# Performance work log

Hardware: AMD Instinct MI355X
Metric: run time of the kernel (lower is better)

The kernel has to match this reference:

```python
import jax, jax.numpy as jnp
import numpy as np

CH = 256
CQK = CH // 8
B, H, W = 4, 64, 64


def setup_inputs() -> dict:
    key = jax.random.key(0)
    ks = jax.random.split(key, 8)
    s_qk = 1.0 / np.sqrt(CH)  # MSR init for 1x1 conv: std = 1/sqrt(fan_in)
    x = jax.random.normal(ks[0], (B, CH, H, W), dtype=jnp.float32)
    Wq = jax.random.normal(ks[1], (CQK, CH), dtype=jnp.float32) * s_qk
    bq = jnp.zeros((CQK,), dtype=jnp.float32)
    Wk = jax.random.normal(ks[2], (CQK, CH), dtype=jnp.float32) * s_qk
    bk = jnp.zeros((CQK,), dtype=jnp.float32)
    Wv = jax.random.normal(ks[3], (CH, CH), dtype=jnp.float32) * s_qk
    bv = jnp.zeros((CH,), dtype=jnp.float32)
    # NOTE: module inits gamma=0; use a nonzero value so the attention branch is active
    gamma = jnp.float32(0.5) * jnp.ones((1,), dtype=jnp.float32)
    return {"x": x, "Wq": Wq, "bq": bq, "Wk": Wk, "bk": bk, "Wv": Wv, "bv": bv, "gamma": gamma}


def reference(x, Wq, bq, Wk, bk, Wv, bv, gamma):
    b, c, h, w = x.shape
    n = h * w
    xf = x.reshape(b, c, n)  # [B, C, N]
    # 1x1 convs are per-pixel channel projections
    q = jnp.einsum('oc,bcn->bon', Wq, xf) + bq[:, None]  # [B, C/8, N]
    k = jnp.einsum('oc,bcn->bon', Wk, xf) + bk[:, None]  # [B, C/8, N]
    v = jnp.einsum('oc,bcn->bon', Wv, xf) + bv[:, None]  # [B, C, N]
    # scores[b, i, j] = q[:, i] . k[:, j]  (no scaling, as in source)
    att = jax.nn.softmax(jnp.einsum('bci,bcj->bij', q, k), axis=-1)  # [B, N, N]
    out = jnp.einsum('bcj,bij->bci', v, att).reshape(b, c, h, w)
    return x + gamma[0] * out
```

## Files before the change

### kernel.cpp

```cpp
#include <hip/hip_runtime.h>
#include <hip/hip_bf16.h>

typedef unsigned short u16;
typedef __attribute__((ext_vector_type(8))) __bf16 bf16x8;
typedef __attribute__((ext_vector_type(8))) unsigned short u16x8;
typedef __attribute__((ext_vector_type(4))) float f32x4;
typedef __attribute__((ext_vector_type(16))) float f32x16;
typedef __attribute__((ext_vector_type(4))) unsigned int u32x4;
typedef __attribute__((ext_vector_type(2))) unsigned int u32x2;

#define MFMA16(a, b, c) __builtin_amdgcn_mfma_f32_16x16x32_bf16((a), (b), (c), 0, 0, 0)
#define MFMA32(a, b, c) __builtin_amdgcn_mfma_f32_32x32x16_bf16((a), (b), (c), 0, 0, 0)

#define BN 4
#define CH 256
#define CQK 32
#define NPIX 4096

__device__ __forceinline__ u16 f2bf(float f) {
    __hip_bfloat16 h = __float2bfloat16(f);
    return *reinterpret_cast<u16*>(&h);
}

__device__ __forceinline__ unsigned pack2(float a, float b) {
    return (unsigned)f2bf(a) | ((unsigned)f2bf(b) << 16);
}

__device__ __forceinline__ unsigned packtr(float a, float b) {
    return __builtin_amdgcn_perm(__float_as_uint(b), __float_as_uint(a), 0x07060302u);
}

__device__ __forceinline__ float bf2f(u16 v) {
    return __uint_as_float(((unsigned)v) << 16);
}

__device__ __forceinline__ f32x16 zero16() {
    f32x16 z;
#pragma unroll
    for (int i = 0; i < 16; ++i) z[i] = 0.f;
    return z;
}

__device__ __forceinline__ int perm16(int k) {
    return (k & 3) | ((k & 4) << 1) | ((k & 8) >> 1);
}

__global__ void k_transpose(const float* __restrict__ x, u16* __restrict__ xt) {
    __shared__ float xs[64][65];
    int n0 = blockIdx.x * 64, c0 = blockIdx.y * 64, b = blockIdx.z;
    int t = threadIdx.x;
    const float* xp = x + ((size_t)(b * CH + c0)) * NPIX + n0;
#pragma unroll
    for (int it = 0; it < 16; ++it) {
        int idx = it * 256 + t;
        int cc = idx >> 6, nn = idx & 63;
        xs[cc][nn] = xp[(size_t)cc * NPIX + nn];
    }
    __syncthreads();
    u16* op = xt + ((size_t)(b * NPIX + n0)) * CH + c0;
#pragma unroll
    for (int it = 0; it < 16; ++it) {
        int idx = it * 256 + t;
        int nn = idx >> 6, cc = idx & 63;
        op[(size_t)nn * CH + cc] = f2bf(xs[cc][nn]);
    }
}

__global__ void k_wcvt(const float* __restrict__ Wq, const float* __restrict__ Wk,
                       const float* __restrict__ Wv, u16* __restrict__ Wbf) {
    int idx = blockIdx.x * 256 + threadIdx.x;
    int o = idx >> 8, c = idx & 255;
    float v;
    if (o < 32) v = Wq[o * 256 + c];
    else if (o < 64) v = Wk[(o - 32) * 256 + c];
    else v = Wv[(o - 64) * 256 + c];
    Wbf[idx] = f2bf(v);
}

__launch_bounds__(256, 1)
__global__ void k_proj(const u16* __restrict__ Wbf, const u16* __restrict__ xt,
                       const float* __restrict__ bq, const float* __restrict__ bk,
                       const float* __restrict__ bv,
                       u16* __restrict__ qb, u16* __restrict__ kb, u16* __restrict__ vb) {
    int b = blockIdx.y, n0 = blockIdx.x * 64;
    int t = threadIdx.x, w = t >> 6, l = t & 63;
    int lr = l & 15, lg = l >> 4;

    f32x4 acc[5][4];
#pragma unroll
    for (int s = 0; s < 5; ++s)
#pragma unroll
        for (int u = 0; u < 4; ++u) acc[s][u] = f32x4{0.f, 0.f, 0.f, 0.f};

    const u16* xtb = xt + ((size_t)(b * NPIX + n0)) * CH;

#pragma unroll
    for (int kk = 0; kk < 8; ++kk) {
        int kof = kk * 32 + lg * 8;
        bf16x8 af[5], bfr[4];
#pragma unroll
        for (int s = 0; s < 5; ++s) {
            int o = w * 16 + s * 64 + lr;
            af[s] = *reinterpret_cast<const bf16x8*>(Wbf + (size_t)o * 256 + kof);
        }
#pragma unroll
        for (int u = 0; u < 4; ++u) {
            int n = u * 16 + lr;
            bfr[u] = *reinterpret_cast<const bf16x8*>(xtb + (size_t)n * CH + kof);
        }
#pragma unroll
        for (int s = 0; s < 5; ++s)
#pragma unroll
            for (int u = 0; u < 4; ++u) acc[s][u] = MFMA16(af[s], bfr[u], acc[s][u]);
    }

    int lrp = perm16(lr);
#pragma unroll
    for (int s = 0; s < 5; ++s) {
        int o0 = w * 16 + s * 64;
#pragma unroll
        for (int r = 0; r < 4; ++r) {
            int o = o0 + lg * 4 + r;
            float bias = (o < 32) ? bq[o] : (o < 64) ? bk[o - 32] : bv[o - 64];
#pragma unroll
            for (int u = 0; u < 4; ++u) {
                float val = acc[s][u][r] + bias;
                u16 h = f2bf(val);
                if (o < 32) qb[((size_t)b * NPIX + n0 + u * 16 + lr) * CQK + o] = h;
                else if (o < 64) kb[((size_t)b * NPIX + n0 + u * 16 + lr) * CQK + (o - 32)] = h;
                else {
                    int c = o - 64;
                    int jp = (u & 1) * 16 + lrp;
                    int sl = jp >> 3, off = jp & 7;
                    int jps = ((sl ^ ((c >> 1) & 3)) << 3) | off;
                    vb[((size_t)(b * CH + c)) * NPIX + n0 + (u >> 1) * 32 + jps] = h;
                }
            }
        }
    }
}

template <int NCHUNK>
__launch_bounds__(128, 2)
__global__ void k_attn8(const u16* __restrict__ qb, const u16* __restrict__ kb,
                        const u16* __restrict__ vb, const float* __restrict__ x,
                        const float* __restrict__ gamma,
                        u16* __restrict__ pacc, float* __restrict__ plsum,
                        float* __restrict__ out) {
    constexpr int JCH = NPIX / NCHUNK;
    constexpr int NT = JCH / 32;
    int it = blockIdx.x;
    int sc = blockIdx.y;
    int s = sc >> 1, ch = sc & 1;
    int b = blockIdx.z;
    int t = threadIdx.x, w = t >> 6, l = t & 63;
    int lr = l & 31, hi = l >> 5;
    int i0 = it * 128 + w * 64;
    int j0 = s * JCH;

    __shared__ alignas(16) u16 vlds[3][4096];
    __shared__ float lsl[2][64];

    bf16x8 qf[2][2];
#pragma unroll
    for (int is = 0; is < 2; ++is) {
        const u16* qrow = qb + ((size_t)b * NPIX + i0 + is * 32 + lr) * CQK;
        qf[is][0] = *(const bf16x8*)(qrow + hi * 8);
        qf[is][1] = *(const bf16x8*)(qrow + 16 + hi * 8);
    }

    const u16* kbase = kb + (size_t)b * NPIX * CQK;
    const u16* vsrc =
        vb + ((size_t)(b * CH + ch * 128 + w * 64 + (l >> 2))) * NPIX + j0 + (l & 3) * 8;

    f32x16 acc[2][4];
#pragma unroll
    for (int is = 0; is < 2; ++is)
#pragma unroll
        for (int ct = 0; ct < 4; ++ct) acc[is][ct] = zero16();
    float lsum[2] = {0.f, 0.f};

    bf16x8 kc0, kc1;
    auto kload = [&](int tt) {
        const u16* kr = kbase + (size_t)(j0 + tt * 32 + lr) * CQK;
        kc0 = *(const bf16x8*)(kr + hi * 8);
        kc1 = *(const bf16x8*)(kr + 16 + hi * 8);
    };
    auto dma = [&](int buf, int tt) {
#pragma unroll
        for (int mm = 0; mm < 4; ++mm) {
            const u16* src = vsrc + (size_t)mm * 16 * NPIX + tt * 32;
            __builtin_amdgcn_global_load_lds(
                (const __attribute__((address_space(1))) unsigned int*)src,
                (__attribute__((address_space(3))) unsigned int*)(
                    &vlds[buf][(w * 64 + mm * 16) * 32]),
                16, 0, 0);
        }
    };
    auto qkexp = [&](bf16x8 (&pa)[4]) {
#pragma unroll
        for (int is = 0; is < 2; ++is) {
            f32x16 sf = MFMA32(kc0, qf[is][0], zero16());
            sf = MFMA32(kc1, qf[is][1], sf);
            float P[16];
#pragma unroll
            for (int e = 0; e < 16; ++e) {
                P[e] = __expf(sf[e] - 32.0f);
                lsum[is] += P[e];
            }
            u32x4 wa = {packtr(P[0], P[1]), packtr(P[2], P[3]),
                        packtr(P[4], P[5]), packtr(P[6], P[7])};
            u32x4 wc = {packtr(P[8], P[9]), packtr(P[10], P[11]),
                        packtr(P[12], P[13]), packtr(P[14], P[15])};
            pa[is * 2] = __builtin_bit_cast(bf16x8, wa);
            pa[is * 2 + 1] = __builtin_bit_cast(bf16x8, wc);
        }
    };
    auto pv = [&](int buf, bf16x8 (&pa)[4]) {
        const u16* base = &vlds[buf][0];
#pragma unroll
        for (int ct = 0; ct < 4; ++ct) {
            int row = ct * 32 + lr;
            int key = (row >> 1) & 3;
            const u16* rp = base + row * 32;
            bf16x8 vf0 = *(const bf16x8*)(rp + ((hi ^ key) << 3));
            bf16x8 vf1 = *(const bf16x8*)(rp + (((2 + hi) ^ key) << 3));
#pragma unroll
            for (int is = 0; is < 2; ++is) {
                acc[is][ct] = MFMA32(pa[is * 2], vf0, acc[is][ct]);
                acc[is][ct] = MFMA32(pa[is * 2 + 1], vf1, acc[is][ct]);
            }
        }
    };

    bf16x8 paA[4], paB[4];

    dma(0, 0);
    kload(0);
    qkexp(paA);
    kload(1);

    for (int tt = 0; tt < NT - 1; ++tt) {
        dma((tt + 1) % 3, tt + 1);
        qkexp(paB);
        kload(tt + 2 < NT ? tt + 2 : NT - 1);
        asm volatile("s_waitcnt vmcnt(6)" ::: "memory");
        __builtin_amdgcn_s_barrier();
        __builtin_amdgcn_sched_barrier(0);
        pv(tt % 3, paA);
#pragma unroll
        for (int e = 0; e < 4; ++e) paA[e] = paB[e];
    }
    asm volatile("s_waitcnt vmcnt(0)" ::: "memory");
    __builtin_amdgcn_s_barrier();
    __builtin_amdgcn_sched_barrier(0);
    pv((NT - 1) % 3, paA);

    lsum[0] += __shfl_xor(lsum[0], 32);
    lsum[1] += __shfl_xor(lsum[1], 32);

    if constexpr (NCHUNK == 1) {
        float g = gamma[0];
        if (l < 32) {
            lsl[w][l] = g / lsum[0];
        }
        if (l >= 32) lsl[w][l] = 0.f;
        if (l < 32) lsl[w][32 + l] = g / lsum[1];
        asm volatile("s_waitcnt lgkmcnt(0)" ::: "memory");
#pragma unroll
        for (int is = 0; is < 2; ++is)
#pragma unroll
            for (int ct = 0; ct < 4; ++ct) {
                int c = ch * 128 + ct * 32 + lr;
                const float* xp = x + ((size_t)(b * CH + c)) * NPIX + i0;
                float* op = out + ((size_t)(b * CH + c)) * NPIX + i0;
#pragma unroll
                for (int r = 0; r < 16; ++r) {
                    int il = is * 32 + (r & 3) + 8 * (r >> 2) + 4 * hi;
                    op[il] = xp[il] + acc[is][ct][r] * lsl[w][il];
                }
            }
    } else {
        size_t pbase = ((((size_t)s * BN + b) * 32 + it) * 256) * 128;
#pragma unroll
        for (int is = 0; is < 2; ++is)
#pragma unroll
            for (int ct = 0; ct < 4; ++ct) {
                int c = ch * 128 + ct * 32 + lr;
#pragma unroll
                for (int q = 0; q < 4; ++q) {
                    int il0 = w * 64 + is * 32 + 8 * q + 4 * hi;
                    u32x2 pr = {pack2(acc[is][ct][4 * q], acc[is][ct][4 * q + 1]),
                                pack2(acc[is][ct][4 * q + 2], acc[is][ct][4 * q + 3])};
                    *(u32x2*)(pacc + pbase + (size_t)c * 128 + il0) = pr;
                }
            }
        if (ch == 0 && l < 32) {
            size_t lb = (((size_t)s * BN + b) * 32 + it) * 128 + w * 64;
            plsum[lb + l] = lsum[0];
            plsum[lb + 32 + l] = lsum[1];
        }
    }
}

template <int NCHUNK>
__global__ void k_reduce(const u16* __restrict__ pacc, const float* __restrict__ plsum,
                         const float* __restrict__ x, const float* __restrict__ gamma,
                         float* __restrict__ out) {
    int cg = blockIdx.x, it = blockIdx.y, b = blockIdx.z;
    int t = threadIdx.x;
    int c0 = cg * 32;
    __shared__ float invl[128];

    if (t < 128) {
        float lt = 0.f;
#pragma unroll
        for (int s = 0; s < NCHUNK; ++s)
            lt += plsum[(((size_t)s * BN + b) * 32 + it) * 128 + t];
        invl[t] = gamma[0] / lt;
    }
    __syncthreads();

    const size_t chunk_stride = (size_t)BN * 32 * 256 * 128;
    size_t base = (((size_t)b * 32 + it) * 256 + c0) * 128;

#pragma unroll
    for (int k = 0; k < 2; ++k) {
        int v = k * 256 + t;
        int cl = v >> 4;
        int io = (v & 15) * 8;
        size_t off = base + (size_t)cl * 128 + io;
        f32x4 a0 = {0.f, 0.f, 0.f, 0.f}, a1 = a0;
#pragma unroll
        for (int s = 0; s < NCHUNK; ++s) {
            u16x8 p = *(const u16x8*)(pacc + (size_t)s * chunk_stride + off);
            a0[0] += bf2f(p[0]); a0[1] += bf2f(p[1]); a0[2] += bf2f(p[2]); a0[3] += bf2f(p[3]);
            a1[0] += bf2f(p[4]); a1[1] += bf2f(p[5]); a1[2] += bf2f(p[6]); a1[3] += bf2f(p[7]);
        }
        f32x4 i0v = *(const f32x4*)(&invl[io]);
        f32x4 i1v = *(const f32x4*)(&invl[io + 4]);
        size_t oi = ((size_t)(b * CH + c0 + cl)) * NPIX + it * 128 + io;
        f32x4 x0 = *(const f32x4*)(x + oi);
        f32x4 x1 = *(const f32x4*)(x + oi + 4);
        *(f32x4*)(out + oi) = x0 + a0 * i0v;
        *(f32x4*)(out + oi + 4) = x1 + a1 * i1v;
    }
}

extern "C" void kernel_launch(void* const* d_in, const int* in_sizes, int n_in,
                              void* d_out, int out_size, void* d_ws, size_t ws_size,
                              hipStream_t stream) {
    const float* x = (const float*)d_in[0];
    const float* Wq = (const float*)d_in[1];
    const float* bq = (const float*)d_in[2];
    const float* Wk = (const float*)d_in[3];
    const float* bk = (const float*)d_in[4];
    const float* Wv = (const float*)d_in[5];
    const float* bv = (const float*)d_in[6];
    const float* gamma = (const float*)d_in[7];
    float* out = (float*)d_out;

    char* ws = (char*)d_ws;
    u16* xt = (u16*)(ws);
    u16* Wbf = (u16*)(ws + 8388608);
    u16* qb = (u16*)(ws + 8388608 + 163840);
    u16* kb = (u16*)(ws + 8388608 + 163840 + 1048576);
    u16* vb = (u16*)(ws + 8388608 + 163840 + 2097152);
    const size_t base_end = 8388608 + 163840 + 2097152 + 8388608;
    u16* pacc = (u16*)(ws + base_end);

    hipLaunchKernelGGL(k_transpose, dim3(64, 4, 4), dim3(256), 0, stream, x, xt);
    hipLaunchKernelGGL(k_wcvt, dim3(320), dim3(256), 0, stream, Wq, Wk, Wv, Wbf);
    hipLaunchKernelGGL(k_proj, dim3(64, 4), dim3(256), 0, stream, Wbf, xt, bq, bk, bv, qb, kb, vb);

    const size_t pacc4 = (size_t)4 * BN * NPIX * CH * 2;
    const size_t pls4 = (size_t)4 * BN * NPIX * 4;

    if (ws_size >= base_end + pacc4 + pls4) {
        float* plsum = (float*)(ws + base_end + pacc4);
        hipLaunchKernelGGL(k_attn8<4>, dim3(32, 8, 4), dim3(128), 0, stream,
                           qb, kb, vb, x, gamma, pacc, plsum, out);
        hipLaunchKernelGGL(k_reduce<4>, dim3(8, 32, 4), dim3(256), 0, stream,
                           pacc, plsum, x, gamma, out);
    } else {
        hipLaunchKernelGGL(k_attn8<1>, dim3(32, 2, 4), dim3(128), 0, stream,
                           qb, kb, vb, x, gamma, pacc, (float*)pacc, out);
    }
}
```

Measured before the change: 94.57 us.

## Halve query rows per wave, use exp2 with prescaled Q, widen V swizzle

The attention kernel now processes 32 query rows per wave instead of 64, doubling the grid and raising launch bounds to 3 blocks per CU. The goal is fewer accumulator registers and more occupancy to hide the latency of K/V loads and exp. Q is prescaled by log2(e) in the projection so the softmax uses exp2f with an equivalent shift. The V LDS swizzle changes from 8-element to 4-element granularity over 8 slots, with reads done as 64-bit pieces. The cost is that K/V tiles are reloaded and re-DMA'd twice as often per query, and each MFMA pair now reuses its V operand fragments less.

```diff
diff --git a/kernel.cpp b/kernel.cpp
--- a/kernel.cpp
+++ b/kernel.cpp
@@ -16,6 +16,9 @@
 #define CH 256
 #define CQK 32
 #define NPIX 4096
+
+#define LOG2E 1.44269504088896f
+#define SHIFT2 46.1662413084468f
 
 __device__ __forceinline__ u16 f2bf(float f) {
     __hip_bfloat16 h = __float2bfloat16(f);
@@ -125,15 +128,16 @@
 #pragma unroll
             for (int u = 0; u < 4; ++u) {
                 float val = acc[s][u][r] + bias;
-                u16 h = f2bf(val);
-                if (o < 32) qb[((size_t)b * NPIX + n0 + u * 16 + lr) * CQK + o] = h;
-                else if (o < 64) kb[((size_t)b * NPIX + n0 + u * 16 + lr) * CQK + (o - 32)] = h;
-                else {
+                if (o < 32) {
+                    qb[((size_t)b * NPIX + n0 + u * 16 + lr) * CQK + o] = f2bf(val * LOG2E);
+                } else if (o < 64) {
+                    kb[((size_t)b * NPIX + n0 + u * 16 + lr) * CQK + (o - 32)] = f2bf(val);
+                } else {
                     int c = o - 64;
                     int jp = (u & 1) * 16 + lrp;
-                    int sl = jp >> 3, off = jp & 7;
-                    int jps = ((sl ^ ((c >> 1) & 3)) << 3) | off;
-                    vb[((size_t)(b * CH + c)) * NPIX + n0 + (u >> 1) * 32 + jps] = h;
+                    int s8 = jp >> 2, rem = jp & 3;
+                    int jps = ((s8 ^ ((c >> 1) & 7)) << 2) | rem;
+                    vb[((size_t)(b * CH + c)) * NPIX + n0 + (u >> 1) * 32 + jps] = f2bf(val);
                 }
             }
         }
@@ -141,44 +145,38 @@
 }
 
 template <int NCHUNK>
-__launch_bounds__(128, 2)
-__global__ void k_attn8(const u16* __restrict__ qb, const u16* __restrict__ kb,
+__launch_bounds__(128, 3)
+__global__ void k_attn9(const u16* __restrict__ qb, const u16* __restrict__ kb,
                         const u16* __restrict__ vb, const float* __restrict__ x,
                         const float* __restrict__ gamma,
                         u16* __restrict__ pacc, float* __restrict__ plsum,
                         float* __restrict__ out) {
     constexpr int JCH = NPIX / NCHUNK;
     constexpr int NT = JCH / 32;
-    int it = blockIdx.x;
+    int itp = blockIdx.x;
     int sc = blockIdx.y;
     int s = sc >> 1, ch = sc & 1;
     int b = blockIdx.z;
     int t = threadIdx.x, w = t >> 6, l = t & 63;
     int lr = l & 31, hi = l >> 5;
-    int i0 = it * 128 + w * 64;
+    int i0 = itp * 64 + w * 32;
     int j0 = s * JCH;
 
     __shared__ alignas(16) u16 vlds[3][4096];
-    __shared__ float lsl[2][64];
-
-    bf16x8 qf[2][2];
-#pragma unroll
-    for (int is = 0; is < 2; ++is) {
-        const u16* qrow = qb + ((size_t)b * NPIX + i0 + is * 32 + lr) * CQK;
-        qf[is][0] = *(const bf16x8*)(qrow + hi * 8);
-        qf[is][1] = *(const bf16x8*)(qrow + 16 + hi * 8);
-    }
+    __shared__ float lsl[2][32];
+
+    const u16* qrow = qb + ((size_t)b * NPIX + i0 + lr) * CQK;
+    bf16x8 qf0 = *(const bf16x8*)(qrow + hi * 8);
+    bf16x8 qf1 = *(const bf16x8*)(qrow + 16 + hi * 8);
 
     const u16* kbase = kb + (size_t)b * NPIX * CQK;
     const u16* vsrc =
         vb + ((size_t)(b * CH + ch * 128 + w * 64 + (l >> 2))) * NPIX + j0 + (l & 3) * 8;
 
-    f32x16 acc[2][4];
-#pragma unroll
-    for (int is = 0; is < 2; ++is)
-#pragma unroll
-        for (int ct = 0; ct < 4; ++ct) acc[is][ct] = zero16();
-    float lsum[2] = {0.f, 0.f};
+    f32x16 acc[4];
+#pragma unroll
+    for (int ct = 0; ct < 4; ++ct) acc[ct] = zero16();
+    float lsum = 0.f;
 
     bf16x8 kc0, kc1;
     auto kload = [&](int tt) {
@@ -197,108 +195,99 @@
                 16, 0, 0);
         }
     };
-    auto qkexp = [&](bf16x8 (&pa)[4]) {
-#pragma unroll
-        for (int is = 0; is < 2; ++is) {
-            f32x16 sf = MFMA32(kc0, qf[is][0], zero16());
-            sf = MFMA32(kc1, qf[is][1], sf);
-            float P[16];
-#pragma unroll
-            for (int e = 0; e < 16; ++e) {
-                P[e] = __expf(sf[e] - 32.0f);
-                lsum[is] += P[e];
-            }
-            u32x4 wa = {packtr(P[0], P[1]), packtr(P[2], P[3]),
-                        packtr(P[4], P[5]), packtr(P[6], P[7])};
-            u32x4 wc = {packtr(P[8], P[9]), packtr(P[10], P[11]),
-                        packtr(P[12], P[13]), packtr(P[14], P[15])};
-            pa[is * 2] = __builtin_bit_cast(bf16x8, wa);
-            pa[is * 2 + 1] = __builtin_bit_cast(bf16x8, wc);
-        }
+    auto qkexp = [&](bf16x8& pa0, bf16x8& pa1) {
+        f32x16 sf = MFMA32(kc0, qf0, zero16());
+        sf = MFMA32(kc1, qf1, sf);
+        float P[16];
+#pragma unroll
+        for (int e = 0; e < 16; ++e) {
+            P[e] = exp2f(sf[e] - SHIFT2);
+            lsum += P[e];
+        }
+        u32x4 wa = {packtr(P[0], P[1]), packtr(P[2], P[3]),
+                    packtr(P[4], P[5]), packtr(P[6], P[7])};
+        u32x4 wc = {packtr(P[8], P[9]), packtr(P[10], P[11]),
+                    packtr(P[12], P[13]), packtr(P[14], P[15])};
+        pa0 = __builtin_bit_cast(bf16x8, wa);
+        pa1 = __builtin_bit_cast(bf16x8, wc);
     };
-    auto pv = [&](int buf, bf16x8 (&pa)[4]) {
+    auto pv = [&](int buf, bf16x8 pa0, bf16x8 pa1) {
         const u16* base = &vlds[buf][0];
 #pragma unroll
         for (int ct = 0; ct < 4; ++ct) {
             int row = ct * 32 + lr;
-            int key = (row >> 1) & 3;
-            const u16* rp = base + row * 32;
-            bf16x8 vf0 = *(const bf16x8*)(rp + ((hi ^ key) << 3));
-            bf16x8 vf1 = *(const bf16x8*)(rp + (((2 + hi) ^ key) << 3));
-#pragma unroll
-            for (int is = 0; is < 2; ++is) {
-                acc[is][ct] = MFMA32(pa[is * 2], vf0, acc[is][ct]);
-                acc[is][ct] = MFMA32(pa[is * 2 + 1], vf1, acc[is][ct]);
-            }
+            int key = (row >> 1) & 7;
+            const u32x2* rp = (const u32x2*)(base + row * 32);
+            u32x2 e0 = rp[(2 * hi) ^ key];
+            u32x2 e1 = rp[(2 * hi + 1) ^ key];
+            u32x2 e2 = rp[(4 + 2 * hi) ^ key];
+            u32x2 e3 = rp[(5 + 2 * hi) ^ key];
+            u32x4 v0 = {e0[0], e0[1], e1[0], e1[1]};
+            u32x4 v1 = {e2[0], e2[1], e3[0], e3[1]};
+            bf16x8 vf0 = __builtin_bit_cast(bf16x8, v0);
+            bf16x8 vf1 = __builtin_bit_cast(bf16x8, v1);
+            acc[ct] = MFMA32(pa0, vf0, acc[ct]);
+            acc[ct] = MFMA32(pa1, vf1, acc[ct]);
         }
     };
 
-    bf16x8 paA[4], paB[4];
+    bf16x8 paA0, paA1, paB0, paB1;
 
     dma(0, 0);
     kload(0);
-    qkexp(paA);
+    qkexp(paA0, paA1);
     kload(1);
 
     for (int tt = 0; tt < NT - 1; ++tt) {
         dma((tt + 1) % 3, tt + 1);
-        qkexp(paB);
+        qkexp(paB0, paB1);
         kload(tt + 2 < NT ? tt + 2 : NT - 1);
         asm volatile("s_waitcnt vmcnt(6)" ::: "memory");
         __builtin_amdgcn_s_barrier();
         __builtin_amdgcn_sched_barrier(0);
-        pv(tt % 3, paA);
-#pragma unroll
-        for (int e = 0; e < 4; ++e) paA[e] = paB[e];
+        pv(tt % 3, paA0, paA1);
+        paA0 = paB0;
+        paA1 = paB1;
     }
     asm volatile("s_waitcnt vmcnt(0)" ::: "memory");
     __builtin_amdgcn_s_barrier();
     __builtin_amdgcn_sched_barrier(0);
-    pv((NT - 1) % 3, paA);
-
-    lsum[0] += __shfl_xor(lsum[0], 32);
-    lsum[1] += __shfl_xor(lsum[1], 32);
+    pv((NT - 1) % 3, paA0, paA1);
+
+    lsum += __shfl_xor(lsum, 32);
 
     if constexpr (NCHUNK == 1) {
         float g = gamma[0];
-        if (l < 32) {
-            lsl[w][l] = g / lsum[0];
-        }
-        if (l >= 32) lsl[w][l] = 0.f;
-        if (l < 32) lsl[w][32 + l] = g / lsum[1];
+        if (l < 32) lsl[w][l] = g / lsum;
         asm volatile("s_waitcnt lgkmcnt(0)" ::: "memory");
-#pragma unroll
-        for (int is = 0; is < 2; ++is)
-#pragma unroll
-            for (int ct = 0; ct < 4; ++ct) {
-                int c = ch * 128 + ct * 32 + lr;
-                const float* xp = x + ((size_t)(b * CH + c)) * NPIX + i0;
-                float* op = out + ((size_t)(b * CH + c)) * NPIX + i0;
-#pragma unroll
-                for (int r = 0; r < 16; ++r) {
-                    int il = is * 32 + (r & 3) + 8 * (r >> 2) + 4 * hi;
-                    op[il] = xp[il] + acc[is][ct][r] * lsl[w][il];
-                }
+        __builtin_amdgcn_s_barrier();
+#pragma unroll
+        for (int ct = 0; ct < 4; ++ct) {
+            int c = ch * 128 + ct * 32 + lr;
+            const float* xp = x + ((size_t)(b * CH + c)) * NPIX + i0;
+            float* op = out + ((size_t)(b * CH + c)) * NPIX + i0;
+#pragma unroll
+            for (int r = 0; r < 16; ++r) {
+                int il = (r & 3) + 8 * (r >> 2) + 4 * hi;
+                op[il] = xp[il] + acc[ct][r] * lsl[w][il];
             }
+        }
     } else {
-        size_t pbase = ((((size_t)s * BN + b) * 32 + it) * 256) * 128;
-#pragma unroll
-        for (int is = 0; is < 2; ++is)
-#pragma unroll
-            for (int ct = 0; ct < 4; ++ct) {
-                int c = ch * 128 + ct * 32 + lr;
-#pragma unroll
-                for (int q = 0; q < 4; ++q) {
-                    int il0 = w * 64 + is * 32 + 8 * q + 4 * hi;
-                    u32x2 pr = {pack2(acc[is][ct][4 * q], acc[is][ct][4 * q + 1]),
-                                pack2(acc[is][ct][4 * q + 2], acc[is][ct][4 * q + 3])};
-                    *(u32x2*)(pacc + pbase + (size_t)c * 128 + il0) = pr;
-                }
+        size_t pbase = ((((size_t)s * BN + b) * 32 + (itp >> 1)) * 256) * 128;
+        int ibase = (itp & 1) * 64 + w * 32;
+#pragma unroll
+        for (int ct = 0; ct < 4; ++ct) {
+            int c = ch * 128 + ct * 32 + lr;
+#pragma unroll
+            for (int q = 0; q < 4; ++q) {
+                int il0 = ibase + 8 * q + 4 * hi;
+                u32x2 pr = {pack2(acc[ct][4 * q], acc[ct][4 * q + 1]),
+                            pack2(acc[ct][4 * q + 2], acc[ct][4 * q + 3])};
+                *(u32x2*)(pacc + pbase + (size_t)c * 128 + il0) = pr;
             }
+        }
         if (ch == 0 && l < 32) {
-            size_t lb = (((size_t)s * BN + b) * 32 + it) * 128 + w * 64;
-            plsum[lb + l] = lsum[0];
-            plsum[lb + 32 + l] = lsum[1];
+            plsum[(((size_t)s * BN + b) * 32 + (itp >> 1)) * 128 + ibase + l] = lsum;
         }
     }
 }
@@ -378,12 +367,12 @@
 
     if (ws_size >= base_end + pacc4 + pls4) {
         float* plsum = (float*)(ws + base_end + pacc4);
-        hipLaunchKernelGGL(k_attn8<4>, dim3(32, 8, 4), dim3(128), 0, stream,
+        hipLaunchKernelGGL(k_attn9<4>, dim3(64, 8, 4), dim3(128), 0, stream,
                            qb, kb, vb, x, gamma, pacc, plsum, out);
         hipLaunchKernelGGL(k_reduce<4>, dim3(8, 32, 4), dim3(256), 0, stream,
                            pacc, plsum, x, gamma, out);
     } else {
-        hipLaunchKernelGGL(k_attn8<1>, dim3(32, 2, 4), dim3(128), 0, stream,
+        hipLaunchKernelGGL(k_attn9<1>, dim3(64, 2, 4), dim3(128), 0, stream,
                            qb, kb, vb, x, gamma, pacc, (float*)pacc, out);
     }
 }
```

Measured after the change: 120.7 us. 1.28x slower.

## Double attention j-tile to 64 with double-buffered V LDS and 8-way swizzle

Applied to the files above, without the earlier changes.

The attention kernel now processes 64 keys per iteration instead of 32. The V tile moves from a triple buffer to a double buffer of twice the size, with a barrier at the end of each iteration. The V layout written by the projection kernel changes to an 8-group XOR swizzle at 4-element granularity, and the PV loop reads V as 8-byte pieces. Raising wave priority around the PV MFMAs with s_setprio aims to cut loop overhead and barrier count per key. The trade-off is losing the previous one-tile-ahead softmax overlap and adding a second barrier each iteration.

```diff
diff --git a/kernel.cpp b/kernel.cpp
--- a/kernel.cpp
+++ b/kernel.cpp
@@ -131,8 +131,8 @@
                 else {
                     int c = o - 64;
                     int jp = (u & 1) * 16 + lrp;
-                    int sl = jp >> 3, off = jp & 7;
-                    int jps = ((sl ^ ((c >> 1) & 3)) << 3) | off;
+                    int s8 = jp >> 2, rem = jp & 3;
+                    int jps = ((s8 ^ ((c >> 1) & 7)) << 2) | rem;
                     vb[((size_t)(b * CH + c)) * NPIX + n0 + (u >> 1) * 32 + jps] = h;
                 }
             }
@@ -142,13 +142,13 @@
 
 template <int NCHUNK>
 __launch_bounds__(128, 2)
-__global__ void k_attn8(const u16* __restrict__ qb, const u16* __restrict__ kb,
-                        const u16* __restrict__ vb, const float* __restrict__ x,
-                        const float* __restrict__ gamma,
-                        u16* __restrict__ pacc, float* __restrict__ plsum,
-                        float* __restrict__ out) {
+__global__ void k_attn10(const u16* __restrict__ qb, const u16* __restrict__ kb,
+                         const u16* __restrict__ vb, const float* __restrict__ x,
+                         const float* __restrict__ gamma,
+                         u16* __restrict__ pacc, float* __restrict__ plsum,
+                         float* __restrict__ out) {
     constexpr int JCH = NPIX / NCHUNK;
-    constexpr int NT = JCH / 32;
+    constexpr int NT = JCH / 64;
     int it = blockIdx.x;
     int sc = blockIdx.y;
     int s = sc >> 1, ch = sc & 1;
@@ -158,7 +158,7 @@
     int i0 = it * 128 + w * 64;
     int j0 = s * JCH;
 
-    __shared__ alignas(16) u16 vlds[3][4096];
+    __shared__ alignas(16) u16 vlds[2][8192];
     __shared__ float lsl[2][64];
 
     bf16x8 qf[2][2];
@@ -170,103 +170,116 @@
     }
 
     const u16* kbase = kb + (size_t)b * NPIX * CQK;
-    const u16* vsrc =
-        vb + ((size_t)(b * CH + ch * 128 + w * 64 + (l >> 2))) * NPIX + j0 + (l & 3) * 8;
+    const u16* vsrc = vb + ((size_t)(b * CH + ch * 128 + w * 64 + (l >> 3))) * NPIX +
+                      j0 + ((l >> 2) & 1) * 32 + (l & 3) * 8;
 
     f32x16 acc[2][4];
 #pragma unroll
     for (int is = 0; is < 2; ++is)
 #pragma unroll
         for (int ct = 0; ct < 4; ++ct) acc[is][ct] = zero16();
-    float lsum[2] = {0.f, 0.f};
-
-    bf16x8 kc0, kc1;
+    float lsum[2][2] = {{0.f, 0.f}, {0.f, 0.f}};
+
+    bf16x8 kc[4];
     auto kload = [&](int tt) {
-        const u16* kr = kbase + (size_t)(j0 + tt * 32 + lr) * CQK;
-        kc0 = *(const bf16x8*)(kr + hi * 8);
-        kc1 = *(const bf16x8*)(kr + 16 + hi * 8);
+#pragma unroll
+        for (int jsub = 0; jsub < 2; ++jsub) {
+            const u16* kr = kbase + (size_t)(j0 + tt * 64 + jsub * 32 + lr) * CQK;
+            kc[2 * jsub] = *(const bf16x8*)(kr + hi * 8);
+            kc[2 * jsub + 1] = *(const bf16x8*)(kr + 16 + hi * 8);
+        }
     };
     auto dma = [&](int buf, int tt) {
 #pragma unroll
-        for (int mm = 0; mm < 4; ++mm) {
-            const u16* src = vsrc + (size_t)mm * 16 * NPIX + tt * 32;
+        for (int mm = 0; mm < 8; ++mm) {
+            const u16* src = vsrc + (size_t)mm * 8 * NPIX + tt * 64;
             __builtin_amdgcn_global_load_lds(
                 (const __attribute__((address_space(1))) unsigned int*)src,
                 (__attribute__((address_space(3))) unsigned int*)(
-                    &vlds[buf][(w * 64 + mm * 16) * 32]),
+                    &vlds[buf][(w * 64 + mm * 8) * 64]),
                 16, 0, 0);
         }
     };
-    auto qkexp = [&](bf16x8 (&pa)[4]) {
-#pragma unroll
-        for (int is = 0; is < 2; ++is) {
-            f32x16 sf = MFMA32(kc0, qf[is][0], zero16());
-            sf = MFMA32(kc1, qf[is][1], sf);
-            float P[16];
-#pragma unroll
-            for (int e = 0; e < 16; ++e) {
-                P[e] = __expf(sf[e] - 32.0f);
-                lsum[is] += P[e];
+    auto qkexp = [&](bf16x8 (&pa)[2][4]) {
+#pragma unroll
+        for (int jsub = 0; jsub < 2; ++jsub)
+#pragma unroll
+            for (int is = 0; is < 2; ++is) {
+                f32x16 sf = MFMA32(kc[2 * jsub], qf[is][0], zero16());
+                sf = MFMA32(kc[2 * jsub + 1], qf[is][1], sf);
+                float P[16];
+#pragma unroll
+                for (int e = 0; e < 16; ++e) {
+                    P[e] = __expf(sf[e] - 32.0f);
+                    lsum[is][jsub] += P[e];
+                }
+                u32x4 wa = {packtr(P[0], P[1]), packtr(P[2], P[3]),
+                            packtr(P[4], P[5]), packtr(P[6], P[7])};
+                u32x4 wc = {packtr(P[8], P[9]), packtr(P[10], P[11]),
+                            packtr(P[12], P[13]), packtr(P[14], P[15])};
+                pa[jsub][is * 2] = __builtin_bit_cast(bf16x8, wa);
+                pa[jsub][is * 2 + 1] = __builtin_bit_cast(bf16x8, wc);
             }
-            u32x4 wa = {packtr(P[0], P[1]), packtr(P[2], P[3]),
-                        packtr(P[4], P[5]), packtr(P[6], P[7])};
-            u32x4 wc = {packtr(P[8], P[9]), packtr(P[10], P[11]),
-                        packtr(P[12], P[13]), packtr(P[14], P[15])};
-            pa[is * 2] = __builtin_bit_cast(bf16x8, wa);
-            pa[is * 2 + 1] = __builtin_bit_cast(bf16x8, wc);
-        }
     };
-    auto pv = [&](int buf, bf16x8 (&pa)[4]) {
+    auto pv = [&](int buf, bf16x8 (&pa)[2][4]) {
         const u16* base = &vlds[buf][0];
-#pragma unroll
-        for (int ct = 0; ct < 4; ++ct) {
-            int row = ct * 32 + lr;
-            int key = (row >> 1) & 3;
-            const u16* rp = base + row * 32;
-            bf16x8 vf0 = *(const bf16x8*)(rp + ((hi ^ key) << 3));
-            bf16x8 vf1 = *(const bf16x8*)(rp + (((2 + hi) ^ key) << 3));
-#pragma unroll
-            for (int is = 0; is < 2; ++is) {
-                acc[is][ct] = MFMA32(pa[is * 2], vf0, acc[is][ct]);
-                acc[is][ct] = MFMA32(pa[is * 2 + 1], vf1, acc[is][ct]);
+        __builtin_amdgcn_s_setprio(1);
+#pragma unroll
+        for (int jsub = 0; jsub < 2; ++jsub)
+#pragma unroll
+            for (int ct = 0; ct < 4; ++ct) {
+                int row = ct * 32 + lr;
+                int key = (row >> 1) & 7;
+                const u32x2* rp = (const u32x2*)(base + row * 64 + jsub * 32);
+                u32x2 e0 = rp[(2 * hi) ^ key];
+                u32x2 e1 = rp[(2 * hi + 1) ^ key];
+                u32x2 e2 = rp[(4 + 2 * hi) ^ key];
+                u32x2 e3 = rp[(5 + 2 * hi) ^ key];
+                u32x4 v0 = {e0[0], e0[1], e1[0], e1[1]};
+                u32x4 v1 = {e2[0], e2[1], e3[0], e3[1]};
+                bf16x8 vf0 = __builtin_bit_cast(bf16x8, v0);
+                bf16x8 vf1 = __builtin_bit_cast(bf16x8, v1);
+#pragma unroll
+                for (int is = 0; is < 2; ++is) {
+                    acc[is][ct] = MFMA32(pa[jsub][is * 2], vf0, acc[is][ct]);
+                    acc[is][ct] = MFMA32(pa[jsub][is * 2 + 1], vf1, acc[is][ct]);
+                }
             }
-        }
+        __builtin_amdgcn_s_setprio(0);
     };
-
-    bf16x8 paA[4], paB[4];
 
     dma(0, 0);
     kload(0);
-    qkexp(paA);
-    kload(1);
-
-    for (int tt = 0; tt < NT - 1; ++tt) {
-        dma((tt + 1) % 3, tt + 1);
-        qkexp(paB);
-        kload(tt + 2 < NT ? tt + 2 : NT - 1);
-        asm volatile("s_waitcnt vmcnt(6)" ::: "memory");
+
+    for (int tt = 0; tt < NT; ++tt) {
+        bf16x8 pa[2][4];
+        if (tt + 1 < NT) dma((tt + 1) & 1, tt + 1);
+        qkexp(pa);
+        if (tt + 1 < NT) kload(tt + 1);
+        if (tt + 1 < NT) {
+            asm volatile("s_waitcnt vmcnt(12)" ::: "memory");
+        } else {
+            asm volatile("s_waitcnt vmcnt(0)" ::: "memory");
+        }
         __builtin_amdgcn_s_barrier();
         __builtin_amdgcn_sched_barrier(0);
-        pv(tt % 3, paA);
-#pragma unroll
-        for (int e = 0; e < 4; ++e) paA[e] = paB[e];
-    }
-    asm volatile("s_waitcnt vmcnt(0)" ::: "memory");
-    __builtin_amdgcn_s_barrier();
-    __builtin_amdgcn_sched_barrier(0);
-    pv((NT - 1) % 3, paA);
-
-    lsum[0] += __shfl_xor(lsum[0], 32);
-    lsum[1] += __shfl_xor(lsum[1], 32);
+        pv(tt & 1, pa);
+        __builtin_amdgcn_s_barrier();
+    }
+
+    float ls0 = lsum[0][0] + lsum[0][1];
+    float ls1 = lsum[1][0] + lsum[1][1];
+    ls0 += __shfl_xor(ls0, 32);
+    ls1 += __shfl_xor(ls1, 32);
 
     if constexpr (NCHUNK == 1) {
         float g = gamma[0];
         if (l < 32) {
-            lsl[w][l] = g / lsum[0];
-        }
-        if (l >= 32) lsl[w][l] = 0.f;
-        if (l < 32) lsl[w][32 + l] = g / lsum[1];
+            lsl[w][l] = g / ls0;
+            lsl[w][32 + l] = g / ls1;
+        }
         asm volatile("s_waitcnt lgkmcnt(0)" ::: "memory");
+        __builtin_amdgcn_s_barrier();
 #pragma unroll
         for (int is = 0; is < 2; ++is)
 #pragma unroll
@@ -297,8 +310,8 @@
             }
         if (ch == 0 && l < 32) {
             size_t lb = (((size_t)s * BN + b) * 32 + it) * 128 + w * 64;
-            plsum[lb + l] = lsum[0];
-            plsum[lb + 32 + l] = lsum[1];
+            plsum[lb + l] = ls0;
+            plsum[lb + 32 + l] = ls1;
         }
     }
 }
@@ -378,12 +391,12 @@
 
     if (ws_size >= base_end + pacc4 + pls4) {
         float* plsum = (float*)(ws + base_end + pacc4);
-        hipLaunchKernelGGL(k_attn8<4>, dim3(32, 8, 4), dim3(128), 0, stream,
+        hipLaunchKernelGGL(k_attn10<4>, dim3(32, 8, 4), dim3(128), 0, stream,
                            qb, kb, vb, x, gamma, pacc, plsum, out);
         hipLaunchKernelGGL(k_reduce<4>, dim3(8, 32, 4), dim3(256), 0, stream,
                            pacc, plsum, x, gamma, out);
     } else {
-        hipLaunchKernelGGL(k_attn8<1>, dim3(32, 2, 4), dim3(128), 0, stream,
+        hipLaunchKernelGGL(k_attn10<1>, dim3(32, 2, 4), dim3(128), 0, stream,
                            qb, kb, vb, x, gamma, pacc, (float*)pacc, out);
     }
 }
```

Result: slower. 118.5 us (+25.3%).
